# Kernel tuning notes

Measured on AMD Instinct MI355X. Metric: run time of the kernel, lower is better.

The kernel has to match this reference:

```python
import jax, jax.numpy as jnp
import numpy as np

B_, L_, D_, E_, N_, DT_, K_ = 2, 1024, 1024, 2048, 16, 64, 4
EPS = 1e-5


def setup_inputs() -> dict:
    key = jax.random.key(0)
    ks = jax.random.split(key, 16)
    s = lambda *sh: 1.0 / np.sqrt(sh[-1])
    return {
        "resid": jax.random.normal(ks[0], (B_, L_, D_), jnp.float32),
        "norm_w": jnp.ones((D_,), jnp.float32),
        "skip_w": jax.random.normal(ks[1], (E_, D_), jnp.float32) * s(E_, D_),
        "in_w": jax.random.normal(ks[2], (E_, D_), jnp.float32) * s(E_, D_),
        "conv_w": jax.random.normal(ks[3], (E_, K_), jnp.float32) * s(E_, K_),
        "conv_b": jax.random.normal(ks[4], (E_,), jnp.float32) * 0.1,
        "wd1": jax.random.normal(ks[5], (DT_, E_), jnp.float32) * s(DT_, E_),
        "wd2": jax.random.normal(ks[6], (E_, DT_), jnp.float32) * s(E_, DT_),
        "wd2_b": jax.random.normal(ks[7], (E_,), jnp.float32) * 0.1,
        "wb": jax.random.normal(ks[8], (N_, E_), jnp.float32) * s(N_, E_),
        "wc": jax.random.normal(ks[9], (N_, E_), jnp.float32) * s(N_, E_),
        "A_log": jnp.log(jax.random.uniform(ks[10], (E_, N_), jnp.float32, 0.5, 4.0)),
        "W_D": jnp.ones((E_,), jnp.float32),
        "out_w": jax.random.normal(ks[11], (D_, E_), jnp.float32) * s(D_, E_),
    }


def _forward(resid, norm_w, skip_w, in_w, conv_w, conv_b, wd1, wd2, wd2_b,
             wb, wc, A_log, W_D, out_w):
    B, L, D = resid.shape
    E, N = A_log.shape
    K = conv_w.shape[-1]
    # RMSNorm
    xn = resid * jax.lax.rsqrt(jnp.mean(resid * resid, -1, keepdims=True) + EPS) * norm_w
    skip = jnp.einsum('bld,ed->ble', xn, skip_w)
    x = jnp.einsum('bld,ed->ble', xn, in_w)
    # causal depthwise conv1d (torch pads both sides by K-1, output cut to [:L])
    xp = jnp.pad(x, ((0, 0), (K - 1, 0), (0, 0)))
    conv = conv_b + sum(xp[:, k:k + L, :] * conv_w[:, k] for k in range(K))
    x = jax.nn.silu(conv)  # [B,L,E] ssm input
    # input-dependent projections
    delta = jax.nn.softplus(jnp.einsum('ble,re->blr', x, wd1) @ wd2.T + wd2_b)  # [B,L,E]
    Bt = jnp.einsum('ble,ne->bln', x, wb)  # [B,L,N]
    Ct = jnp.einsum('ble,ne->bln', x, wc)  # [B,L,N]
    A = -jnp.exp(A_log)  # [E,N]

    def step(h, inp):
        dt, b_t, c_t, x_t = inp  # [B,E],[B,N],[B,N],[B,E]
        A_bar = jnp.exp(dt[:, :, None] * A)          # [B,E,N]
        h = A_bar * h + (dt * x_t)[:, :, None] * b_t[:, None, :]
        y = jnp.einsum('ben,bn->be', h, c_t)
        return h, y

    h0 = jnp.zeros((B, E, N), x.dtype)
    xs = (delta.transpose(1, 0, 2), Bt.transpose(1, 0, 2),
          Ct.transpose(1, 0, 2), x.transpose(1, 0, 2))
    _, y = jax.lax.scan(step, h0, xs)
    y = y.transpose(1, 0, 2)  # [B,L,E]
    y = y + x * W_D
    y = y * jax.nn.silu(skip)
    y = jnp.einsum('ble,de->bld', y, out_w)
    return resid + y


def reference(resid, norm_w, skip_w, in_w, conv_w, conv_b, wd1, wd2, wd2_b,
              wb, wc, A_log, W_D, out_w):
    return _forward(resid, norm_w, skip_w, in_w, conv_w, conv_b, wd1, wd2,
                    wd2_b, wb, wc, A_log, W_D, out_w)
```

## Files before the change

### kernel.cpp

```cpp
#include <hip/hip_runtime.h>
#include <cstdint>

typedef unsigned short u16;
typedef float f32x4 __attribute__((ext_vector_type(4)));
typedef __bf16 bf16x8 __attribute__((ext_vector_type(8)));
typedef u16 u16x8 __attribute__((ext_vector_type(8)));

__device__ __forceinline__ u16 f2bf(float f) {
  uint32_t u = __float_as_uint(f);
  u += 0x7fffu + ((u >> 16) & 1u);
  return (u16)(u >> 16);
}
__device__ __forceinline__ float bf2f(u16 s) {
  return __uint_as_float(((uint32_t)s) << 16);
}

__device__ __forceinline__ void ld16(const u16* g, u16* l) {
  auto* gp = reinterpret_cast<const __attribute__((address_space(1))) u16*>(
      reinterpret_cast<uintptr_t>(g));
  auto* lp = reinterpret_cast<__attribute__((address_space(3))) u16*>(
      static_cast<uint32_t>(reinterpret_cast<uintptr_t>(l)));
  __builtin_amdgcn_global_load_lds(gp, lp, 16, 0, 0);
}

__device__ __forceinline__ f32x4 mfma16(u16x8 a, u16x8 b, f32x4 c) {
  return __builtin_amdgcn_mfma_f32_16x16x32_bf16(
      __builtin_bit_cast(bf16x8, a), __builtin_bit_cast(bf16x8, b), c, 0, 0, 0);
}

__device__ __forceinline__ float sigmoidf_(float x) { return 1.f / (1.f + __expf(-x)); }
__device__ __forceinline__ float siluf_(float x) { return x * sigmoidf_(x); }
__device__ __forceinline__ float softplusf_(float x) {
  return fmaxf(x, 0.f) + log1pf(__expf(-fabsf(x)));
}

#define PACK_TOT 6651904
__global__ __launch_bounds__(256) void pack_kernel(
    const float* __restrict__ skip_w, const float* __restrict__ in_w,
    const float* __restrict__ out_w, const float* __restrict__ wd2,
    const float* __restrict__ wd1, const float* __restrict__ wb,
    const float* __restrict__ wc, const float* __restrict__ A_log,
    u16* __restrict__ skipw_bf, u16* __restrict__ inw_bf, u16* __restrict__ outw_bf,
    u16* __restrict__ wd2_bf, u16* __restrict__ w96, float* __restrict__ Aneg) {
  int stride = gridDim.x * 256;
  for (int i = blockIdx.x * 256 + threadIdx.x; i < PACK_TOT; i += stride) {
    int j = i;
    if (j < 2097152) { skipw_bf[j] = f2bf(skip_w[j]); continue; } j -= 2097152;
    if (j < 2097152) { inw_bf[j] = f2bf(in_w[j]); continue; } j -= 2097152;
    if (j < 2097152) { outw_bf[j] = f2bf(out_w[j]); continue; } j -= 2097152;
    if (j < 131072)  { wd2_bf[j] = f2bf(wd2[j]); continue; } j -= 131072;
    if (j < 131072)  { w96[j] = f2bf(wd1[j]); continue; } j -= 131072;
    if (j < 32768)   { w96[131072 + j] = f2bf(wb[j]); continue; } j -= 32768;
    if (j < 32768)   { w96[163840 + j] = f2bf(wc[j]); continue; } j -= 32768;
    Aneg[j] = -__expf(A_log[j]);
  }
}

__global__ __launch_bounds__(256) void rmsnorm_kernel(
    const float* __restrict__ x, const float* __restrict__ w, u16* __restrict__ out) {
  int row = blockIdx.x, t = threadIdx.x;
  const float4* xr = (const float4*)(x + (size_t)row * 1024);
  float4 v = xr[t];
  float ss = v.x * v.x + v.y * v.y + v.z * v.z + v.w * v.w;
  for (int o = 32; o > 0; o >>= 1) ss += __shfl_xor(ss, o);
  __shared__ float wsum[4];
  if ((t & 63) == 0) wsum[t >> 6] = ss;
  __syncthreads();
  float tot = wsum[0] + wsum[1] + wsum[2] + wsum[3];
  float rs = rsqrtf(tot * (1.0f / 1024.0f) + 1e-5f);
  float4 wv = ((const float4*)w)[t];
  uint2 pk;
  pk.x = (uint32_t)f2bf(v.x * rs * wv.x) | ((uint32_t)f2bf(v.y * rs * wv.y) << 16);
  pk.y = (uint32_t)f2bf(v.z * rs * wv.z) | ((uint32_t)f2bf(v.w * rs * wv.w) << 16);
  ((uint2*)out)[row * 256 + t] = pk;
}

template <int BM, int BN, int EPI>
__global__ __launch_bounds__(256) void gemm_bt(
    const u16* __restrict__ A, const u16* __restrict__ B0, const u16* __restrict__ B1,
    int M, int N, int K, int Nsplit,
    void* __restrict__ C0, void* __restrict__ C1,
    const float* __restrict__ bias, const float* __restrict__ addsrc) {
  constexpr int TM = BM / 32, TN = BN / 32;
  __shared__ __align__(16) u16 sA[BM * 32];
  __shared__ __align__(16) u16 sB[BN * 32];
  const int t = threadIdx.x;
  const int lane = t & 63, wid = t >> 6;
  const int wm = wid >> 1, wn = wid & 1;
  const int mBase = blockIdx.y * BM;
  const int nBase = blockIdx.x * BN;
  const bool hi = (nBase >= Nsplit);
  const u16* Bp = hi ? B1 : B0;
  const int nB0 = nBase - (hi ? Nsplit : 0);
  const int col = lane & 15, quad = lane >> 4;

  f32x4 acc[TM][TN];
#pragma unroll
  for (int i = 0; i < TM; ++i)
#pragma unroll
    for (int j = 0; j < TN; ++j) acc[i][j] = f32x4{0.f, 0.f, 0.f, 0.f};

  for (int k0 = 0; k0 < K; k0 += 32) {
#pragma unroll
    for (int c = t; c < BM * 4; c += 256) {
      int row = c >> 2, k8 = (c & 3) * 8;
      ld16(A + (size_t)(mBase + row) * K + k0 + k8, &sA[c * 8]);
    }
#pragma unroll
    for (int c = t; c < BN * 4; c += 256) {
      int row = c >> 2, k8 = (c & 3) * 8;
      ld16(Bp + (size_t)(nB0 + row) * K + k0 + k8, &sB[c * 8]);
    }
    __syncthreads();
    u16x8 af[TM], bfv[TN];
#pragma unroll
    for (int i = 0; i < TM; ++i)
      af[i] = *(const u16x8*)&sA[(wm * (BM / 2) + i * 16 + col) * 32 + quad * 8];
#pragma unroll
    for (int j = 0; j < TN; ++j)
      bfv[j] = *(const u16x8*)&sB[(wn * (BN / 2) + j * 16 + col) * 32 + quad * 8];
#pragma unroll
    for (int i = 0; i < TM; ++i)
#pragma unroll
      for (int j = 0; j < TN; ++j) acc[i][j] = mfma16(af[i], bfv[j], acc[i][j]);
    __syncthreads();
  }

#pragma unroll
  for (int i = 0; i < TM; ++i) {
#pragma unroll
    for (int j = 0; j < TN; ++j) {
#pragma unroll
      for (int r = 0; r < 4; ++r) {
        int gm = mBase + wm * (BM / 2) + i * 16 + quad * 4 + r;
        int gn = nBase + wn * (BN / 2) + j * 16 + col;
        float v = acc[i][j][r];
        if (EPI == 0) {
          if (gn < Nsplit)
            ((u16*)C0)[(size_t)gm * Nsplit + gn] = f2bf(v);
          else
            ((float*)C1)[(size_t)gm * (N - Nsplit) + (gn - Nsplit)] = v;
        } else if (EPI == 1) {
          ((float*)C0)[(size_t)gm * N + gn] = softplusf_(v + bias[gn]);
        } else {
          ((float*)C0)[(size_t)gm * N + gn] = addsrc[(size_t)gm * N + gn] + v;
        }
      }
    }
  }
}

__global__ __launch_bounds__(256) void gemm_skinny_splitk(
    const u16* __restrict__ A, const u16* __restrict__ B,
    float* __restrict__ part) {
  __shared__ __align__(16) u16 sA[64 * 32];
  __shared__ __align__(16) u16 sB[96 * 32];
  const int t = threadIdx.x, lane = t & 63, w = t >> 6;
  const int mBase = blockIdx.x * 64;
  const int kBase = blockIdx.y * 256;
  const int col = lane & 15, quad = lane >> 4;
  const int K = 2048;
  f32x4 acc[6];
#pragma unroll
  for (int j = 0; j < 6; ++j) acc[j] = f32x4{0.f, 0.f, 0.f, 0.f};

  for (int k0 = kBase; k0 < kBase + 256; k0 += 32) {
    for (int c = t; c < 640; c += 256) {
      if (c < 256) {
        int row = c >> 2, k8 = (c & 3) * 8;
        ld16(A + (size_t)(mBase + row) * K + k0 + k8, &sA[c * 8]);
      } else {
        int cb = c - 256;
        int row = cb >> 2, k8 = (cb & 3) * 8;
        ld16(B + (size_t)row * K + k0 + k8, &sB[cb * 8]);
      }
    }
    __syncthreads();
    u16x8 af = *(const u16x8*)&sA[(w * 16 + col) * 32 + quad * 8];
#pragma unroll
    for (int j = 0; j < 6; ++j) {
      u16x8 bfv = *(const u16x8*)&sB[(j * 16 + col) * 32 + quad * 8];
      acc[j] = mfma16(af, bfv, acc[j]);
    }
    __syncthreads();
  }
  float* pp = part + (size_t)blockIdx.y * (2048 * 96);
#pragma unroll
  for (int j = 0; j < 6; ++j)
#pragma unroll
    for (int r = 0; r < 4; ++r) {
      int gm = mBase + w * 16 + quad * 4 + r;
      int gn = j * 16 + col;
      pp[gm * 96 + gn] = acc[j][r];
    }
}

__global__ __launch_bounds__(256) void skinny_reduce(
    const float* __restrict__ part, u16* __restrict__ d1_bf,
    float* __restrict__ bc) {
  int i = blockIdx.x * 256 + threadIdx.x;
  float s = 0.f;
#pragma unroll
  for (int kc = 0; kc < 8; ++kc) s += part[kc * 196608 + i];
  int m = i / 96, n = i - m * 96;
  if (n < 64) d1_bf[m * 64 + n] = f2bf(s);
  else bc[m * 32 + n - 64] = s;
}

__global__ __launch_bounds__(256) void conv_silu_kernel(
    const float* __restrict__ xin, const float* __restrict__ conv_w,
    const float* __restrict__ conv_b, float* __restrict__ xconv,
    u16* __restrict__ xconv_bf) {
  int i = blockIdx.x * 256 + threadIdx.x;
  int e = i & 2047;
  int l = (i >> 11) & 1023;
  float4 wv = ((const float4*)conv_w)[e];
  float acc = conv_b[e] + xin[i] * wv.w;
  if (l >= 1) acc += xin[i - 2048] * wv.z;
  if (l >= 2) acc += xin[i - 4096] * wv.y;
  if (l >= 3) acc += xin[i - 6144] * wv.x;
  float s = siluf_(acc);
  xconv[i] = s;
  xconv_bf[i] = f2bf(s);
}

__global__ __launch_bounds__(256) void scan1_kernel(
    const float* __restrict__ delta, const float* __restrict__ xconv,
    const float* __restrict__ bc, const float* __restrict__ Aneg,
    float* __restrict__ hloc, float* __restrict__ Ssum) {
  int t = threadIdx.x;
  int e = blockIdx.x * 256 + t;
  int c = blockIdx.y, b = blockIdx.z;
  int m0 = b * 1024 + c * 32;
  __shared__ float sBC[1024];
  for (int j = t; j < 1024; j += 256) sBC[j] = bc[m0 * 32 + j];
  float Ar[16], h[16];
#pragma unroll
  for (int n = 0; n < 16; ++n) { Ar[n] = Aneg[e * 16 + n]; h[n] = 0.f; }
  float S = 0.f;
  __syncthreads();
  for (int l = 0; l < 32; ++l) {
    size_t m = (size_t)(m0 + l) * 2048 + e;
    float dt = delta[m], xv = xconv[m];
    S += dt;
    float dx = dt * xv;
    const float* bl = &sBC[l * 32];
#pragma unroll
    for (int n = 0; n < 16; ++n) h[n] = __expf(dt * Ar[n]) * h[n] + dx * bl[n];
  }
  size_t base = ((size_t)(b * 32 + c) * 2048 + e) * 16;
#pragma unroll
  for (int n = 0; n < 16; ++n) hloc[base + n] = h[n];
  Ssum[(b * 32 + c) * 2048 + e] = S;
}

__global__ __launch_bounds__(256) void combine_kernel(
    const float* __restrict__ Aneg, const float* __restrict__ Ssum,
    float* __restrict__ hloc) {
  int tid = blockIdx.x * 256 + threadIdx.x;
  int b = tid >> 15, r = tid & 32767;
  int e = r >> 4;
  float a = Aneg[r];
  float h = 0.f;
  for (int c = 0; c < 32; ++c) {
    size_t base = (size_t)(b * 32 + c) * 32768 + r;
    float hl = hloc[base];
    float S = Ssum[(b * 32 + c) * 2048 + e];
    hloc[base] = h;
    h = __expf(a * S) * h + hl;
  }
}

__global__ __launch_bounds__(256) void scan2_kernel(
    const float* __restrict__ delta, const float* __restrict__ xconv,
    const float* __restrict__ bc, const float* __restrict__ Aneg,
    const float* __restrict__ hloc, const u16* __restrict__ skip_bf,
    const float* __restrict__ W_D, u16* __restrict__ yfin_bf) {
  int t = threadIdx.x;
  int e = blockIdx.x * 256 + t;
  int c = blockIdx.y, b = blockIdx.z;
  int m0 = b * 1024 + c * 32;
  __shared__ float sBC[1024];
  for (int j = t; j < 1024; j += 256) sBC[j] = bc[m0 * 32 + j];
  float Ar[16], h[16];
  size_t hbase = ((size_t)(b * 32 + c) * 2048 + e) * 16;
#pragma unroll
  for (int n = 0; n < 16; ++n) { Ar[n] = Aneg[e * 16 + n]; h[n] = hloc[hbase + n]; }
  float wd = W_D[e];
  __syncthreads();
  for (int l = 0; l < 32; ++l) {
    size_t m = (size_t)(m0 + l) * 2048 + e;
    float dt = delta[m], xv = xconv[m];
    float dx = dt * xv;
    const float* bl = &sBC[l * 32];
    float y = 0.f;
#pragma unroll
    for (int n = 0; n < 16; ++n) {
      h[n] = __expf(dt * Ar[n]) * h[n] + dx * bl[n];
      y += h[n] * bl[16 + n];
    }
    float yv = y + xv * wd;
    float sk = bf2f(skip_bf[m]);
    yv *= sk * sigmoidf_(sk);
    yfin_bf[m] = f2bf(yv);
  }
}

extern "C" void kernel_launch(void* const* d_in, const int* in_sizes, int n_in,
                              void* d_out, int out_size, void* d_ws, size_t ws_size,
                              hipStream_t stream) {
  (void)in_sizes; (void)n_in; (void)out_size; (void)ws_size;
  const float* resid  = (const float*)d_in[0];
  const float* norm_w = (const float*)d_in[1];
  const float* skip_w = (const float*)d_in[2];
  const float* in_w   = (const float*)d_in[3];
  const float* conv_w = (const float*)d_in[4];
  const float* conv_b = (const float*)d_in[5];
  const float* wd1    = (const float*)d_in[6];
  const float* wd2    = (const float*)d_in[7];
  const float* wd2_b  = (const float*)d_in[8];
  const float* wb     = (const float*)d_in[9];
  const float* wc     = (const float*)d_in[10];
  const float* A_log  = (const float*)d_in[11];
  const float* W_D    = (const float*)d_in[12];
  const float* out_w  = (const float*)d_in[13];

  char* p = (char*)d_ws;
  u16*   skipw_bf = (u16*)(p + 0);
  u16*   inw_bf   = (u16*)(p + 4194304);
  u16*   outw_bf  = (u16*)(p + 8388608);
  u16*   wd2_bf   = (u16*)(p + 12582912);
  u16*   w96      = (u16*)(p + 12845056);
  float* Aneg     = (float*)(p + 13238272);
  u16*   xn_bf    = (u16*)(p + 13369344);
  u16*   skip_bf  = (u16*)(p + 17563648);
  float* xin      = (float*)(p + 25952256);
  float* xconv    = (float*)(p + 42729472);
  u16*   xconv_bf = (u16*)(p + 59506688);
  u16*   d1_bf    = (u16*)(p + 67895296);
  float* bc       = (float*)(p + 68157440);
  u16*   yfin_bf  = (u16*)(p + 68419584);
  float* hloc     = (float*)(p + 76808192);
  float* Ssum     = (float*)(p + 85196800);
  float* delta    = xin;
  float* part     = hloc;

  pack_kernel<<<8192, 256, 0, stream>>>(skip_w, in_w, out_w, wd2, wd1, wb, wc, A_log,
                                        skipw_bf, inw_bf, outw_bf, wd2_bf, w96, Aneg);
  rmsnorm_kernel<<<2048, 256, 0, stream>>>(resid, norm_w, xn_bf);
  gemm_bt<128, 128, 0><<<dim3(32, 16), 256, 0, stream>>>(
      xn_bf, skipw_bf, inw_bf, 2048, 4096, 1024, 2048,
      (void*)skip_bf, (void*)xin, nullptr, nullptr);
  conv_silu_kernel<<<16384, 256, 0, stream>>>(xin, conv_w, conv_b, xconv, xconv_bf);
  gemm_skinny_splitk<<<dim3(32, 8), 256, 0, stream>>>(xconv_bf, w96, part);
  skinny_reduce<<<768, 256, 0, stream>>>(part, d1_bf, bc);
  gemm_bt<128, 128, 1><<<dim3(16, 16), 256, 0, stream>>>(
      d1_bf, wd2_bf, wd2_bf, 2048, 2048, 64, 2048,
      (void*)delta, nullptr, wd2_b, nullptr);
  scan1_kernel<<<dim3(8, 32, 2), 256, 0, stream>>>(delta, xconv, bc, Aneg, hloc, Ssum);
  combine_kernel<<<256, 256, 0, stream>>>(Aneg, Ssum, hloc);
  scan2_kernel<<<dim3(8, 32, 2), 256, 0, stream>>>(delta, xconv, bc, Aneg, hloc,
                                                   skip_bf, W_D, yfin_bf);
  gemm_bt<64, 64, 2><<<dim3(16, 32), 256, 0, stream>>>(
      yfin_bf, outw_bf, outw_bf, 2048, 1024, 2048, 1024,
      (void*)d_out, nullptr, nullptr, resid);
}
```

Baseline: 270.1 us.

## Store intermediate activations in bf16 and add BK template to GEMM

```diff
diff --git a/kernel.cpp b/kernel.cpp
--- a/kernel.cpp
+++ b/kernel.cpp
@@ -75,15 +75,16 @@
   ((uint2*)out)[row * 256 + t] = pk;
 }
 
-template <int BM, int BN, int EPI>
+template <int BM, int BN, int BK, int EPI>
 __global__ __launch_bounds__(256) void gemm_bt(
     const u16* __restrict__ A, const u16* __restrict__ B0, const u16* __restrict__ B1,
     int M, int N, int K, int Nsplit,
     void* __restrict__ C0, void* __restrict__ C1,
     const float* __restrict__ bias, const float* __restrict__ addsrc) {
   constexpr int TM = BM / 32, TN = BN / 32;
-  __shared__ __align__(16) u16 sA[BM * 32];
-  __shared__ __align__(16) u16 sB[BN * 32];
+  constexpr int KC = BK / 8;
+  __shared__ __align__(16) u16 sA[BM * BK];
+  __shared__ __align__(16) u16 sB[BN * BK];
   const int t = threadIdx.x;
   const int lane = t & 63, wid = t >> 6;
   const int wm = wid >> 1, wn = wid & 1;
@@ -100,29 +101,32 @@
 #pragma unroll
     for (int j = 0; j < TN; ++j) acc[i][j] = f32x4{0.f, 0.f, 0.f, 0.f};
 
-  for (int k0 = 0; k0 < K; k0 += 32) {
-#pragma unroll
-    for (int c = t; c < BM * 4; c += 256) {
-      int row = c >> 2, k8 = (c & 3) * 8;
+  for (int k0 = 0; k0 < K; k0 += BK) {
+#pragma unroll
+    for (int c = t; c < BM * KC; c += 256) {
+      int row = c / KC, k8 = (c % KC) * 8;
       ld16(A + (size_t)(mBase + row) * K + k0 + k8, &sA[c * 8]);
     }
 #pragma unroll
-    for (int c = t; c < BN * 4; c += 256) {
-      int row = c >> 2, k8 = (c & 3) * 8;
+    for (int c = t; c < BN * KC; c += 256) {
+      int row = c / KC, k8 = (c % KC) * 8;
       ld16(Bp + (size_t)(nB0 + row) * K + k0 + k8, &sB[c * 8]);
     }
     __syncthreads();
-    u16x8 af[TM], bfv[TN];
-#pragma unroll
-    for (int i = 0; i < TM; ++i)
-      af[i] = *(const u16x8*)&sA[(wm * (BM / 2) + i * 16 + col) * 32 + quad * 8];
-#pragma unroll
-    for (int j = 0; j < TN; ++j)
-      bfv[j] = *(const u16x8*)&sB[(wn * (BN / 2) + j * 16 + col) * 32 + quad * 8];
-#pragma unroll
-    for (int i = 0; i < TM; ++i)
-#pragma unroll
-      for (int j = 0; j < TN; ++j) acc[i][j] = mfma16(af[i], bfv[j], acc[i][j]);
+#pragma unroll
+    for (int kk = 0; kk < BK / 32; ++kk) {
+      u16x8 af[TM], bfv[TN];
+#pragma unroll
+      for (int i = 0; i < TM; ++i)
+        af[i] = *(const u16x8*)&sA[(wm * (BM / 2) + i * 16 + col) * BK + kk * 32 + quad * 8];
+#pragma unroll
+      for (int j = 0; j < TN; ++j)
+        bfv[j] = *(const u16x8*)&sB[(wn * (BN / 2) + j * 16 + col) * BK + kk * 32 + quad * 8];
+#pragma unroll
+      for (int i = 0; i < TM; ++i)
+#pragma unroll
+        for (int j = 0; j < TN; ++j) acc[i][j] = mfma16(af[i], bfv[j], acc[i][j]);
+    }
     __syncthreads();
   }
 
@@ -139,9 +143,9 @@
           if (gn < Nsplit)
             ((u16*)C0)[(size_t)gm * Nsplit + gn] = f2bf(v);
           else
-            ((float*)C1)[(size_t)gm * (N - Nsplit) + (gn - Nsplit)] = v;
+            ((u16*)C1)[(size_t)gm * (N - Nsplit) + (gn - Nsplit)] = f2bf(v);
         } else if (EPI == 1) {
-          ((float*)C0)[(size_t)gm * N + gn] = softplusf_(v + bias[gn]);
+          ((u16*)C0)[(size_t)gm * N + gn] = f2bf(softplusf_(v + bias[gn]));
         } else {
           ((float*)C0)[(size_t)gm * N + gn] = addsrc[(size_t)gm * N + gn] + v;
         }
@@ -208,24 +212,21 @@
 }
 
 __global__ __launch_bounds__(256) void conv_silu_kernel(
-    const float* __restrict__ xin, const float* __restrict__ conv_w,
-    const float* __restrict__ conv_b, float* __restrict__ xconv,
-    u16* __restrict__ xconv_bf) {
+    const u16* __restrict__ xin_bf, const float* __restrict__ conv_w,
+    const float* __restrict__ conv_b, u16* __restrict__ xconv_bf) {
   int i = blockIdx.x * 256 + threadIdx.x;
   int e = i & 2047;
   int l = (i >> 11) & 1023;
   float4 wv = ((const float4*)conv_w)[e];
-  float acc = conv_b[e] + xin[i] * wv.w;
-  if (l >= 1) acc += xin[i - 2048] * wv.z;
-  if (l >= 2) acc += xin[i - 4096] * wv.y;
-  if (l >= 3) acc += xin[i - 6144] * wv.x;
-  float s = siluf_(acc);
-  xconv[i] = s;
-  xconv_bf[i] = f2bf(s);
+  float acc = conv_b[e] + bf2f(xin_bf[i]) * wv.w;
+  if (l >= 1) acc += bf2f(xin_bf[i - 2048]) * wv.z;
+  if (l >= 2) acc += bf2f(xin_bf[i - 4096]) * wv.y;
+  if (l >= 3) acc += bf2f(xin_bf[i - 6144]) * wv.x;
+  xconv_bf[i] = f2bf(siluf_(acc));
 }
 
 __global__ __launch_bounds__(256) void scan1_kernel(
-    const float* __restrict__ delta, const float* __restrict__ xconv,
+    const u16* __restrict__ delta_bf, const u16* __restrict__ xconv_bf,
     const float* __restrict__ bc, const float* __restrict__ Aneg,
     float* __restrict__ hloc, float* __restrict__ Ssum) {
   int t = threadIdx.x;
@@ -241,7 +242,7 @@
   __syncthreads();
   for (int l = 0; l < 32; ++l) {
     size_t m = (size_t)(m0 + l) * 2048 + e;
-    float dt = delta[m], xv = xconv[m];
+    float dt = bf2f(delta_bf[m]), xv = bf2f(xconv_bf[m]);
     S += dt;
     float dx = dt * xv;
     const float* bl = &sBC[l * 32];
@@ -272,7 +273,7 @@
 }
 
 __global__ __launch_bounds__(256) void scan2_kernel(
-    const float* __restrict__ delta, const float* __restrict__ xconv,
+    const u16* __restrict__ delta_bf, const u16* __restrict__ xconv_bf,
     const float* __restrict__ bc, const float* __restrict__ Aneg,
     const float* __restrict__ hloc, const u16* __restrict__ skip_bf,
     const float* __restrict__ W_D, u16* __restrict__ yfin_bf) {
@@ -290,7 +291,7 @@
   __syncthreads();
   for (int l = 0; l < 32; ++l) {
     size_t m = (size_t)(m0 + l) * 2048 + e;
-    float dt = delta[m], xv = xconv[m];
+    float dt = bf2f(delta_bf[m]), xv = bf2f(xconv_bf[m]);
     float dx = dt * xv;
     const float* bl = &sBC[l * 32];
     float y = 0.f;
@@ -334,34 +335,34 @@
   float* Aneg     = (float*)(p + 13238272);
   u16*   xn_bf    = (u16*)(p + 13369344);
   u16*   skip_bf  = (u16*)(p + 17563648);
-  float* xin      = (float*)(p + 25952256);
-  float* xconv    = (float*)(p + 42729472);
-  u16*   xconv_bf = (u16*)(p + 59506688);
-  u16*   d1_bf    = (u16*)(p + 67895296);
-  float* bc       = (float*)(p + 68157440);
-  u16*   yfin_bf  = (u16*)(p + 68419584);
-  float* hloc     = (float*)(p + 76808192);
-  float* Ssum     = (float*)(p + 85196800);
-  float* delta    = xin;
-  float* part     = hloc;
+  u16*   xin_bf   = (u16*)(p + 25952256);
+  u16*   xconv_bf = (u16*)(p + 34340864);
+  u16*   delta_bf = (u16*)(p + 42729472);
+  u16*   d1_bf    = (u16*)(p + 51118080);
+  float* bc       = (float*)(p + 51380224);
+  u16*   yfin_bf  = (u16*)(p + 51642368);
+  float* part     = (float*)(p + 60030976);
+  float* hloc     = (float*)(p + 66322432);
+  float* Ssum     = (float*)(p + 74711040);
 
   pack_kernel<<<8192, 256, 0, stream>>>(skip_w, in_w, out_w, wd2, wd1, wb, wc, A_log,
                                         skipw_bf, inw_bf, outw_bf, wd2_bf, w96, Aneg);
   rmsnorm_kernel<<<2048, 256, 0, stream>>>(resid, norm_w, xn_bf);
-  gemm_bt<128, 128, 0><<<dim3(32, 16), 256, 0, stream>>>(
+  gemm_bt<128, 128, 32, 0><<<dim3(32, 16), 256, 0, stream>>>(
       xn_bf, skipw_bf, inw_bf, 2048, 4096, 1024, 2048,
-      (void*)skip_bf, (void*)xin, nullptr, nullptr);
-  conv_silu_kernel<<<16384, 256, 0, stream>>>(xin, conv_w, conv_b, xconv, xconv_bf);
+      (void*)skip_bf, (void*)xin_bf, nullptr, nullptr);
+  conv_silu_kernel<<<16384, 256, 0, stream>>>(xin_bf, conv_w, conv_b, xconv_bf);
   gemm_skinny_splitk<<<dim3(32, 8), 256, 0, stream>>>(xconv_bf, w96, part);
   skinny_reduce<<<768, 256, 0, stream>>>(part, d1_bf, bc);
-  gemm_bt<128, 128, 1><<<dim3(16, 16), 256, 0, stream>>>(
+  gemm_bt<128, 128, 64, 1><<<dim3(16, 16), 256, 0, stream>>>(
       d1_bf, wd2_bf, wd2_bf, 2048, 2048, 64, 2048,
-      (void*)delta, nullptr, wd2_b, nullptr);
-  scan1_kernel<<<dim3(8, 32, 2), 256, 0, stream>>>(delta, xconv, bc, Aneg, hloc, Ssum);
+      (void*)delta_bf, nullptr, wd2_b, nullptr);
+  scan1_kernel<<<dim3(8, 32, 2), 256, 0, stream>>>(delta_bf, xconv_bf, bc, Aneg,
+                                                   hloc, Ssum);
   combine_kernel<<<256, 256, 0, stream>>>(Aneg, Ssum, hloc);
-  scan2_kernel<<<dim3(8, 32, 2), 256, 0, stream>>>(delta, xconv, bc, Aneg, hloc,
+  scan2_kernel<<<dim3(8, 32, 2), 256, 0, stream>>>(delta_bf, xconv_bf, bc, Aneg, hloc,
                                                    skip_bf, W_D, yfin_bf);
-  gemm_bt<64, 64, 2><<<dim3(16, 32), 256, 0, stream>>>(
+  gemm_bt<64, 64, 64, 2><<<dim3(16, 32), 256, 0, stream>>>(
       yfin_bf, outw_bf, outw_bf, 2048, 1024, 2048, 1024,
       (void*)d_out, nullptr, nullptr, resid);
 }
```

Result: faster. 262.0 us (-3.0%).
